# Optimization experiments

Hardware: AMD Instinct MI355X
Metric: run time of the kernel (lower is better)

Reference implementation:

```python
import jax, jax.numpy as jnp
import numpy as np

N = 20000       # nodes
E = 160000      # edges (avg degree 8)
NFEAT = 512
NHID = 512
NCLASS = 64
NLAYERS = 4


def setup_inputs() -> dict:
    key = jax.random.key(0)
    ks = jax.random.split(key, 9)
    s = 0.05
    x = jax.random.normal(ks[0], (N, NFEAT), dtype=jnp.float32)
    edge_index = jax.random.randint(ks[1], (2, E), 0, N, dtype=jnp.int64)
    W_enc = jax.random.normal(ks[2], (NFEAT, NHID), dtype=jnp.float32) * s
    b_enc = jnp.zeros((NHID,), dtype=jnp.float32)
    W_convs = jax.random.normal(ks[3], (NLAYERS, NHID, NHID), dtype=jnp.float32) * s
    b_convs = jnp.zeros((NLAYERS, NHID), dtype=jnp.float32)
    W_dec = jax.random.normal(ks[4], (NHID, NCLASS), dtype=jnp.float32) * s
    b_dec = jnp.zeros((NCLASS,), dtype=jnp.float32)
    return {"x": x, "edge_index": edge_index, "W_enc": W_enc, "b_enc": b_enc,
            "W_convs": W_convs, "b_convs": b_convs, "W_dec": W_dec, "b_dec": b_dec}


def reference(x, edge_index, W_enc, b_enc, W_convs, b_convs, W_dec, b_dec):
    n = x.shape[0]
    loops = jnp.arange(n, dtype=edge_index.dtype)
    # GCNConv adds self-loops, then sym-normalizes: D^-1/2 (A+I) D^-1/2
    src = jnp.concatenate([edge_index[0], loops])  # [E+N]
    dst = jnp.concatenate([edge_index[1], loops])  # [E+N]
    deg = jax.ops.segment_sum(jnp.ones_like(dst, dtype=x.dtype), dst, num_segments=N)
    dinv = jnp.where(deg > 0, jax.lax.rsqrt(deg), jnp.zeros_like(deg))
    norm = (dinv[src] * dinv[dst])[:, None]  # [E+N, 1]

    # encoder: relu(Linear)
    h = jax.nn.relu(x @ W_enc + b_enc)

    def gcn_step(h, wb):
        W, b = wb
        hW = h @ W                                   # [N, H]
        msg = hW[src] * norm                         # gather + scale
        agg = jax.ops.segment_sum(msg, dst, num_segments=N)  # scatter-add
        return jax.nn.relu(agg + b), None            # bias after aggregation (PyG)

    h, _ = jax.lax.scan(gcn_step, h, (W_convs, b_convs))

    # decoder (dropout p=0 in eval -> identity)
    return h @ W_dec + b_dec
```

## Files before the change

### kernel.cpp

```cpp
#include <hip/hip_runtime.h>

#define N_NODES 20000
#define E_EDGES 160000
#define NFEAT   512
#define NHID    512
#define NCLASS  64
#define NLAYERS 4

#define SCAN_CHUNK 1024
#define NBLK ((N_NODES + SCAN_CHUNK - 1) / SCAN_CHUNK)
#define CNT_BLOCKS ((E_EDGES + 255) / 256)
#define CVT_BLOCKS ((N_NODES * NFEAT) / 2048)

using bf16x8 = __attribute__((ext_vector_type(8))) short;
using f32x4  = __attribute__((ext_vector_type(4))) float;
using u16x8  = __attribute__((ext_vector_type(8))) unsigned short;

__device__ __forceinline__ unsigned short f2bf(float f) {
    union { float f; unsigned int u; } v; v.f = f;
    unsigned int u = v.u + 0x7FFFu + ((v.u >> 16) & 1u);
    return (unsigned short)(u >> 16);
}
__device__ __forceinline__ float bf2f(unsigned short h) {
    union { unsigned int u; float f; } v; v.u = ((unsigned int)h) << 16;
    return v.f;
}
__device__ __forceinline__ void gl2lds16(const void* gptr, void* lptr) {
    __builtin_amdgcn_global_load_lds(
        (const __attribute__((address_space(1))) unsigned int*)gptr,
        (__attribute__((address_space(3))) unsigned int*)lptr,
        16, 0, 0);
}

__global__ __launch_bounds__(256) void prep_all(const int* __restrict__ dst,
                                                int* __restrict__ counts,
                                                int* __restrict__ bsums,
                                                const float* __restrict__ W_enc,
                                                const float* __restrict__ W_convs,
                                                const float* __restrict__ W_dec,
                                                unsigned short* __restrict__ WencT,
                                                unsigned short* __restrict__ WcvT,
                                                unsigned short* __restrict__ WdecT,
                                                const float* __restrict__ x,
                                                unsigned short* __restrict__ Xbf) {
    __shared__ int bins[NBLK];
    __shared__ float tile[32][33];
    const int b = blockIdx.x, t = threadIdx.x;

    if (b < CNT_BLOCKS) {
        if (t < NBLK) bins[t] = 0;
        __syncthreads();
        const int e = b * 256 + t;
        if (e < E_EDGES) {
            const int d = dst[e];
            atomicAdd(&counts[d], 1);
            atomicAdd(&bins[d >> 10], 1);
        }
        __syncthreads();
        if (t < NBLK && bins[t]) atomicAdd(&bsums[t], bins[t]);
        return;
    }

    if (b >= CNT_BLOCKS + 6 * 256) {
        const int cid = b - CNT_BLOCKS - 6 * 256;
        const size_t base = (size_t)cid * 2048 + (size_t)t * 8;
        const float4 f0 = *(const float4*)(x + base);
        const float4 f1 = *(const float4*)(x + base + 4);
        u16x8 pk;
        pk[0] = f2bf(f0.x); pk[1] = f2bf(f0.y);
        pk[2] = f2bf(f0.z); pk[3] = f2bf(f0.w);
        pk[4] = f2bf(f1.x); pk[5] = f2bf(f1.y);
        pk[6] = f2bf(f1.z); pk[7] = f2bf(f1.w);
        *(u16x8*)(Xbf + base) = pk;
        return;
    }

    const int bid = b - CNT_BLOCKS;
    const int id  = bid >> 8;
    const int rem = bid & 255;
    const int n0  = (rem & 15) * 32;
    const int k0  = (rem >> 4) * 32;
    const float* W; unsigned short* WT; int N;
    const int K = 512;
    if (id == 0)            { W = W_enc; WT = WencT; N = NHID; }
    else if (id <= NLAYERS) { W = W_convs + (size_t)(id - 1) * NHID * NHID;
                              WT = WcvT  + (size_t)(id - 1) * NHID * NHID; N = NHID; }
    else                    { W = W_dec; WT = WdecT; N = NCLASS; }
    if (n0 >= N) return;
    const int tx = t & 31, ty = t >> 5;
#pragma unroll
    for (int i = 0; i < 32; i += 8)
        tile[ty + i][tx] = W[(size_t)(k0 + ty + i) * N + n0 + tx];
    __syncthreads();
#pragma unroll
    for (int i = 0; i < 32; i += 8)
        WT[(size_t)(n0 + ty + i) * K + k0 + tx] = f2bf(tile[tx][ty + i]);
}

__global__ __launch_bounds__(256) void write_rowptr(const int* __restrict__ counts,
                                                    const int* __restrict__ bsums,
                                                    int* __restrict__ row_ptr,
                                                    int* __restrict__ cursor,
                                                    float* __restrict__ dinv) {
    __shared__ int part[256];
    __shared__ int boff_s;
    const int b = blockIdx.x, t = threadIdx.x;

    if (t < 64) {
        int v = (t < NBLK && t < b) ? bsums[t] : 0;
        for (int off = 32; off > 0; off >>= 1) v += __shfl_xor(v, off, 64);
        if (t == 0) boff_s = v;
    }

    const int base = b * SCAN_CHUNK + t * 4;
    int c[4], s = 0;
    for (int i = 0; i < 4; ++i) {
        int idx = base + i;
        c[i] = (idx < N_NODES) ? counts[idx] : 0;
        s += c[i];
    }
    part[t] = s;
    __syncthreads();
    for (int off = 1; off < 256; off <<= 1) {
        int v = (t >= off) ? part[t - off] : 0;
        __syncthreads();
        part[t] += v;
        __syncthreads();
    }
    int run = boff_s + ((t == 0) ? 0 : part[t - 1]);
    for (int i = 0; i < 4; ++i) {
        int idx = base + i;
        if (idx < N_NODES) {
            row_ptr[idx] = run;
            cursor[idx]  = run;
            dinv[idx]    = rsqrtf((float)c[i] + 1.0f);
            run += c[i];
        }
    }
    if (b == 0 && t == 0) row_ptr[N_NODES] = E_EDGES;
}

__global__ __launch_bounds__(256) void csr_fill(const int* __restrict__ src,
                                                const int* __restrict__ dst,
                                                const float* __restrict__ dinv,
                                                int* __restrict__ cursor,
                                                int2* __restrict__ ew) {
    int e = blockIdx.x * 256 + threadIdx.x;
    if (e < E_EDGES) {
        int s = src[e], d = dst[e];
        int pos = atomicAdd(&cursor[d], 1);
        ew[pos] = make_int2(s, __float_as_int(dinv[s] * dinv[d]));
    }
    if (e < 8) ew[E_EDGES + e] = make_int2(0, 0);
}

template <int BM, int BN, int WR, int WC, bool RELU, bool HASBIAS, bool OUTBF16>
__global__ __launch_bounds__(256) void gemm_mfma(const unsigned short* __restrict__ A,
                                                 const unsigned short* __restrict__ BT,
                                                 const float* __restrict__ bias,
                                                 void* __restrict__ Cout,
                                                 int M, int N, int K) {
    constexpr int BK  = 64;
    constexpr int R   = BM / (16 * WR);
    constexpr int C   = BN / (16 * WC);
    constexpr int RA  = (BM * BK) / (256 * 8);
    constexpr int RB  = (BN * BK) / (256 * 8);
    constexpr int LPT = RA + RB;
    __shared__ unsigned short lA[2][BM * BK];
    __shared__ unsigned short lB[2][BN * BK];

    const int t    = threadIdx.x;
    const int lane = t & 63;
    const int wv   = t >> 6;
    const int wr   = wv / WC;
    const int wc   = wv % WC;
    const int lm   = lane & 15;
    const int quad = lane >> 4;
    const int sw   = lm & 7;

    const int MBLK = (M + BM - 1) / BM;
    const int NBN  = N / BN;
    int mblk, nblk;
    {
        const int i    = blockIdx.x;
        const int full = (MBLK / 8) * 8 * NBN;
        if (i < full) {
            const int g = i / (8 * NBN);
            const int l = i % (8 * NBN);
            mblk = g * 8 + (l & 7);
            nblk = l >> 3;
        } else {
            const int t2  = i - full;
            const int rem = MBLK - (MBLK / 8) * 8;
            mblk = (MBLK / 8) * 8 + t2 % rem;
            nblk = t2 / rem;
        }
    }
    const int m0 = mblk * BM;
    const int n0 = nblk * BN;

    f32x4 acc[R][C] = {};

    auto stage = [&](int s, int kt) {
#pragma unroll
        for (int i = 0; i < RA; ++i) {
            int idx = i * 256 + t;
            int row = idx >> 3;
            int c8  = idx & 7;
            int gr = m0 + row; if (gr >= M) gr = M - 1;
            gl2lds16(A + (size_t)gr * K + kt + (((c8 ^ (row & 7)) << 3)),
                     &lA[s][idx * 8]);
        }
#pragma unroll
        for (int i = 0; i < RB; ++i) {
            int idx = i * 256 + t;
            int row = idx >> 3;
            int c8  = idx & 7;
            gl2lds16(BT + (size_t)(n0 + row) * K + kt + (((c8 ^ (row & 7)) << 3)),
                     &lB[s][idx * 8]);
        }
    };

    stage(0, 0);
    int cur = 0;
    for (int kt = 0; kt < K; kt += BK) {
        if (kt + BK < K) {
            stage(cur ^ 1, kt + BK);
            asm volatile("s_waitcnt vmcnt(%0)" :: "i"(LPT) : "memory");
        } else {
            asm volatile("s_waitcnt vmcnt(0)" ::: "memory");
        }
        __builtin_amdgcn_sched_barrier(0);
        __builtin_amdgcn_s_barrier();

        bf16x8 af[R][2], bfr[C][2];
#pragma unroll
        for (int r = 0; r < R; ++r)
#pragma unroll
            for (int h = 0; h < 2; ++h)
                af[r][h] = *(const bf16x8*)
                    &lA[cur][(wr * R * 16 + r * 16 + lm) * BK +
                             (((h * 4 + quad) ^ sw) << 3)];
#pragma unroll
        for (int c = 0; c < C; ++c)
#pragma unroll
            for (int h = 0; h < 2; ++h)
                bfr[c][h] = *(const bf16x8*)
                    &lB[cur][(wc * C * 16 + c * 16 + lm) * BK +
                             (((h * 4 + quad) ^ sw) << 3)];
        asm volatile("s_waitcnt lgkmcnt(0)" ::: "memory");
        __builtin_amdgcn_sched_barrier(0);
#pragma unroll
        for (int h = 0; h < 2; ++h)
#pragma unroll
            for (int r = 0; r < R; ++r)
#pragma unroll
                for (int c = 0; c < C; ++c)
                    acc[r][c] = __builtin_amdgcn_mfma_f32_16x16x32_bf16(
                        af[r][h], bfr[c][h], acc[r][c], 0, 0, 0);
        __builtin_amdgcn_sched_barrier(0);
        __builtin_amdgcn_s_barrier();
        cur ^= 1;
    }

#pragma unroll
    for (int r = 0; r < R; ++r) {
#pragma unroll
        for (int c = 0; c < C; ++c) {
            const int colg = n0 + wc * C * 16 + c * 16 + lm;
            const float bb = HASBIAS ? bias[colg] : 0.0f;
            const int rowb = m0 + wr * R * 16 + r * 16 + quad * 4;
#pragma unroll
            for (int i = 0; i < 4; ++i) {
                const int rr = rowb + i;
                if (rr < M) {
                    float v = acc[r][c][i] + bb;
                    if (RELU) v = fmaxf(v, 0.0f);
                    if (OUTBF16)
                        ((unsigned short*)Cout)[(size_t)rr * N + colg] = f2bf(v);
                    else
                        ((float*)Cout)[(size_t)rr * N + colg] = v;
                }
            }
        }
    }
}

__global__ __launch_bounds__(256) void gcn_aggregate(const unsigned short* __restrict__ hW,
                                                     const int* __restrict__ row_ptr,
                                                     const int2* __restrict__ ew,
                                                     const float* __restrict__ dinv,
                                                     const float* __restrict__ bias,
                                                     unsigned short* __restrict__ out) {
    const int wv   = threadIdx.x >> 6;
    const int lane = threadIdx.x & 63;
    int d = blockIdx.x * 4 + wv;
    d = __builtin_amdgcn_readfirstlane(d);
    if (d >= N_NODES) return;
    const int beg = __builtin_amdgcn_readfirstlane(row_ptr[d]);
    const int end = __builtin_amdgcn_readfirstlane(row_ptr[d + 1]);
    const size_t foff = (size_t)lane * 8;

    const float di = dinv[d];
    const float sl = di * di;
    u16x8 sv = *(const u16x8*)(hW + (size_t)d * NHID + foff);
    float acc[8];
#pragma unroll
    for (int i = 0; i < 8; ++i) acc[i] = bf2f(sv[i]) * sl;

    for (int j = beg; j < end; j += 8) {
        int   sK[8];
        float wK[8];
        u16x8 v[8];
#pragma unroll
        for (int k = 0; k < 8; ++k) {
            const int jj = j + k;
            const int2 e = ew[jj];
            const bool valid = jj < end;
            sK[k] = valid ? e.x : 0;
            wK[k] = valid ? __int_as_float(e.y) : 0.0f;
        }
#pragma unroll
        for (int k = 0; k < 8; ++k)
            v[k] = *(const u16x8*)(hW + (size_t)sK[k] * NHID + foff);
#pragma unroll
        for (int k = 0; k < 8; ++k)
#pragma unroll
            for (int i = 0; i < 8; ++i)
                acc[i] += bf2f(v[k][i]) * wK[k];
    }

    const float4 b0v = *(const float4*)(bias + foff);
    const float4 b1v = *(const float4*)(bias + foff + 4);
    u16x8 r;
    r[0] = f2bf(fmaxf(acc[0] + b0v.x, 0.0f));
    r[1] = f2bf(fmaxf(acc[1] + b0v.y, 0.0f));
    r[2] = f2bf(fmaxf(acc[2] + b0v.z, 0.0f));
    r[3] = f2bf(fmaxf(acc[3] + b0v.w, 0.0f));
    r[4] = f2bf(fmaxf(acc[4] + b1v.x, 0.0f));
    r[5] = f2bf(fmaxf(acc[5] + b1v.y, 0.0f));
    r[6] = f2bf(fmaxf(acc[6] + b1v.z, 0.0f));
    r[7] = f2bf(fmaxf(acc[7] + b1v.w, 0.0f));
    *(u16x8*)(out + (size_t)d * NHID + foff) = r;
}

extern "C" void kernel_launch(void* const* d_in, const int* in_sizes, int n_in,
                              void* d_out, int out_size, void* d_ws, size_t ws_size,
                              hipStream_t stream) {
    const float* x       = (const float*)d_in[0];
    const int*   ei      = (const int*)d_in[1];
    const float* W_enc   = (const float*)d_in[2];
    const float* b_enc   = (const float*)d_in[3];
    const float* W_convs = (const float*)d_in[4];
    const float* b_convs = (const float*)d_in[5];
    const float* W_dec   = (const float*)d_in[6];
    const float* b_dec   = (const float*)d_in[7];
    float* out = (float*)d_out;

    const int* src = ei;
    const int* dst = ei + E_EDGES;

    char* ws = (char*)d_ws;
    auto alloc = [&](size_t bytes) {
        char* p = ws;
        ws += (bytes + 255) / 256 * 256;
        return p;
    };
    float* dinv     = (float*)alloc(N_NODES * 4);
    int*   counts   = (int*)  alloc((N_NODES + NBLK) * 4);
    int*   bsums    = counts + N_NODES;
    int*   row_ptr  = (int*)  alloc((N_NODES + 1) * 4);
    int*   cursor   = (int*)  alloc(N_NODES * 4);
    int2*  ew       = (int2*) alloc((E_EDGES + 8) * 8);
    unsigned short* WencT = (unsigned short*)alloc((size_t)NFEAT * NHID * 2);
    unsigned short* WcvT  = (unsigned short*)alloc((size_t)NLAYERS * NHID * NHID * 2);
    unsigned short* WdecT = (unsigned short*)alloc((size_t)NHID * NCLASS * 2);
    unsigned short* B1    = (unsigned short*)alloc((size_t)N_NODES * NHID * 2);
    unsigned short* B2    = (unsigned short*)alloc((size_t)N_NODES * NHID * 2);
    unsigned short* Xbf   = B2;

    hipMemsetAsync(counts, 0, (N_NODES + NBLK) * sizeof(int), stream);
    prep_all<<<CNT_BLOCKS + 6 * 256 + CVT_BLOCKS, 256, 0, stream>>>(
        dst, counts, bsums, W_enc, W_convs, W_dec, WencT, WcvT, WdecT, x, Xbf);
    write_rowptr<<<NBLK, 256, 0, stream>>>(counts, bsums, row_ptr, cursor, dinv);
    csr_fill<<<(E_EDGES + 255) / 256, 256, 0, stream>>>(src, dst, dinv, cursor, ew);

    const int MBLK64 = (N_NODES + 63) / 64;

    gemm_mfma<64, 128, 2, 2, true, true, true>
        <<<MBLK64 * (NHID / 128), 256, 0, stream>>>(
        Xbf, WencT, b_enc, B1, N_NODES, NHID, NFEAT);

    for (int L = 0; L < NLAYERS; ++L) {
        gemm_mfma<64, 128, 2, 2, false, false, true>
            <<<MBLK64 * (NHID / 128), 256, 0, stream>>>(
            B1, WcvT + (size_t)L * NHID * NHID, nullptr, B2, N_NODES, NHID, NHID);
        gcn_aggregate<<<(N_NODES + 3) / 4, 256, 0, stream>>>(
            B2, row_ptr, ew, dinv, b_convs + (size_t)L * NHID, B1);
    }

    gemm_mfma<64, 64, 2, 2, false, true, false>
        <<<MBLK64 * (NCLASS / 64), 256, 0, stream>>>(
        B1, WdecT, b_dec, out, N_NODES, NCLASS, NHID);
}
```

Measured before the change: 339.1 us.

## Keep full B panel resident in LDS and stream A fragments from global

Replaces the double-buffered LDS GEMM with a kernel that loads the whole K=512 slice of the weight panel (BN=64 columns, 64KB) into swizzled LDS once. Each wave then reads its own A-row fragments straight from global memory into registers, prefetching one k-step ahead. This removes per-k-tile barriers and the LDS staging of A. In exchange, A reads are uncoalesced 16-byte per-lane global loads with little latency hiding, and the large LDS footprint limits occupancy. Tile shapes change to 256x64 for the hidden GEMMs and 128x64 for the decoder.

```diff
diff --git a/kernel.cpp b/kernel.cpp
--- a/kernel.cpp
+++ b/kernel.cpp
@@ -154,29 +154,22 @@
     if (e < 8) ew[E_EDGES + e] = make_int2(0, 0);
 }
 
-template <int BM, int BN, int WR, int WC, bool RELU, bool HASBIAS, bool OUTBF16>
-__global__ __launch_bounds__(256) void gemm_mfma(const unsigned short* __restrict__ A,
+template <int R, int BN, bool RELU, bool HASBIAS, bool OUTBF16>
+__global__ __launch_bounds__(256) void gemm_bres(const unsigned short* __restrict__ A,
                                                  const unsigned short* __restrict__ BT,
                                                  const float* __restrict__ bias,
                                                  void* __restrict__ Cout,
-                                                 int M, int N, int K) {
-    constexpr int BK  = 64;
-    constexpr int R   = BM / (16 * WR);
-    constexpr int C   = BN / (16 * WC);
-    constexpr int RA  = (BM * BK) / (256 * 8);
-    constexpr int RB  = (BN * BK) / (256 * 8);
-    constexpr int LPT = RA + RB;
-    __shared__ unsigned short lA[2][BM * BK];
-    __shared__ unsigned short lB[2][BN * BK];
+                                                 int M, int N) {
+    constexpr int K  = 512;
+    constexpr int BM = 4 * R * 16;
+    constexpr int C  = BN / 16;
+    __shared__ unsigned short lB[BN * K];
 
     const int t    = threadIdx.x;
     const int lane = t & 63;
     const int wv   = t >> 6;
-    const int wr   = wv / WC;
-    const int wc   = wv % WC;
     const int lm   = lane & 15;
-    const int quad = lane >> 4;
-    const int sw   = lm & 7;
+    const int q    = lane >> 4;
 
     const int MBLK = (M + BM - 1) / BM;
     const int NBN  = N / BN;
@@ -191,7 +184,7 @@
             nblk = l >> 3;
         } else {
             const int t2  = i - full;
-            const int rem = MBLK - (MBLK / 8) * 8;
+            const int rem = MBLK & 7;
             mblk = (MBLK / 8) * 8 + t2 % rem;
             nblk = t2 / rem;
         }
@@ -199,77 +192,61 @@
     const int m0 = mblk * BM;
     const int n0 = nblk * BN;
 
+#pragma unroll
+    for (int i = 0; i < (BN * 64) / 256; ++i) {
+        const int idx = i * 256 + t;
+        const int row = idx >> 6;
+        const int c64 = idx & 63;
+        const int g   = (c64 & ~7) | ((c64 & 7) ^ (row & 7));
+        gl2lds16(BT + (size_t)(n0 + row) * K + g * 8, &lB[idx * 8]);
+    }
+    __syncthreads();
+
+    const unsigned short* ap[R];
+#pragma unroll
+    for (int r = 0; r < R; ++r) {
+        int gr = m0 + wv * R * 16 + r * 16 + lm;
+        if (gr >= M) gr = M - 1;
+        ap[r] = A + (size_t)gr * K + q * 8;
+    }
+
     f32x4 acc[R][C] = {};
-
-    auto stage = [&](int s, int kt) {
-#pragma unroll
-        for (int i = 0; i < RA; ++i) {
-            int idx = i * 256 + t;
-            int row = idx >> 3;
-            int c8  = idx & 7;
-            int gr = m0 + row; if (gr >= M) gr = M - 1;
-            gl2lds16(A + (size_t)gr * K + kt + (((c8 ^ (row & 7)) << 3)),
-                     &lA[s][idx * 8]);
-        }
-#pragma unroll
-        for (int i = 0; i < RB; ++i) {
-            int idx = i * 256 + t;
-            int row = idx >> 3;
-            int c8  = idx & 7;
-            gl2lds16(BT + (size_t)(n0 + row) * K + kt + (((c8 ^ (row & 7)) << 3)),
-                     &lB[s][idx * 8]);
-        }
-    };
-
-    stage(0, 0);
-    int cur = 0;
-    for (int kt = 0; kt < K; kt += BK) {
-        if (kt + BK < K) {
-            stage(cur ^ 1, kt + BK);
-            asm volatile("s_waitcnt vmcnt(%0)" :: "i"(LPT) : "memory");
-        } else {
-            asm volatile("s_waitcnt vmcnt(0)" ::: "memory");
-        }
-        __builtin_amdgcn_sched_barrier(0);
-        __builtin_amdgcn_s_barrier();
-
-        bf16x8 af[R][2], bfr[C][2];
+    bf16x8 aC[R], aN[R];
+#pragma unroll
+    for (int r = 0; r < R; ++r) aC[r] = *(const bf16x8*)ap[r];
+
+    for (int kt = 0; kt < K; kt += 32) {
+        if (kt + 32 < K) {
+#pragma unroll
+            for (int r = 0; r < R; ++r)
+                aN[r] = *(const bf16x8*)(ap[r] + kt + 32);
+        }
+        bf16x8 bf[C];
+        const int cb = kt >> 3;
+#pragma unroll
+        for (int c = 0; c < C; ++c) {
+            const int row  = c * 16 + lm;
+            const int c64  = cb + q;
+            const int phys = (c64 & ~7) | ((c64 & 7) ^ (row & 7));
+            bf[c] = *(const bf16x8*)&lB[row * K + phys * 8];
+        }
 #pragma unroll
         for (int r = 0; r < R; ++r)
 #pragma unroll
-            for (int h = 0; h < 2; ++h)
-                af[r][h] = *(const bf16x8*)
-                    &lA[cur][(wr * R * 16 + r * 16 + lm) * BK +
-                             (((h * 4 + quad) ^ sw) << 3)];
-#pragma unroll
-        for (int c = 0; c < C; ++c)
-#pragma unroll
-            for (int h = 0; h < 2; ++h)
-                bfr[c][h] = *(const bf16x8*)
-                    &lB[cur][(wc * C * 16 + c * 16 + lm) * BK +
-                             (((h * 4 + quad) ^ sw) << 3)];
-        asm volatile("s_waitcnt lgkmcnt(0)" ::: "memory");
-        __builtin_amdgcn_sched_barrier(0);
-#pragma unroll
-        for (int h = 0; h < 2; ++h)
-#pragma unroll
-            for (int r = 0; r < R; ++r)
-#pragma unroll
-                for (int c = 0; c < C; ++c)
-                    acc[r][c] = __builtin_amdgcn_mfma_f32_16x16x32_bf16(
-                        af[r][h], bfr[c][h], acc[r][c], 0, 0, 0);
-        __builtin_amdgcn_sched_barrier(0);
-        __builtin_amdgcn_s_barrier();
-        cur ^= 1;
+            for (int c = 0; c < C; ++c)
+                acc[r][c] = __builtin_amdgcn_mfma_f32_16x16x32_bf16(
+                    aC[r], bf[c], acc[r][c], 0, 0, 0);
+#pragma unroll
+        for (int r = 0; r < R; ++r) aC[r] = aN[r];
     }
 
 #pragma unroll
     for (int r = 0; r < R; ++r) {
 #pragma unroll
         for (int c = 0; c < C; ++c) {
-            const int colg = n0 + wc * C * 16 + c * 16 + lm;
+            const int colg = n0 + c * 16 + lm;
             const float bb = HASBIAS ? bias[colg] : 0.0f;
-            const int rowb = m0 + wr * R * 16 + r * 16 + quad * 4;
+            const int rowb = m0 + wv * R * 16 + r * 16 + q * 4;
 #pragma unroll
             for (int i = 0; i < 4; ++i) {
                 const int rr = rowb + i;
@@ -385,21 +362,22 @@
     write_rowptr<<<NBLK, 256, 0, stream>>>(counts, bsums, row_ptr, cursor, dinv);
     csr_fill<<<(E_EDGES + 255) / 256, 256, 0, stream>>>(src, dst, dinv, cursor, ew);
 
-    const int MBLK64 = (N_NODES + 63) / 64;
-
-    gemm_mfma<64, 128, 2, 2, true, true, true>
-        <<<MBLK64 * (NHID / 128), 256, 0, stream>>>(
-        Xbf, WencT, b_enc, B1, N_NODES, NHID, NFEAT);
+    const int MBLK256 = (N_NODES + 255) / 256;
+    const int MBLK128 = (N_NODES + 127) / 128;
+
+    gemm_bres<4, 64, true, true, true>
+        <<<MBLK256 * (NHID / 64), 256, 0, stream>>>(
+        Xbf, WencT, b_enc, B1, N_NODES, NHID);
 
     for (int L = 0; L < NLAYERS; ++L) {
-        gemm_mfma<64, 128, 2, 2, false, false, true>
-            <<<MBLK64 * (NHID / 128), 256, 0, stream>>>(
-            B1, WcvT + (size_t)L * NHID * NHID, nullptr, B2, N_NODES, NHID, NHID);
+        gemm_bres<4, 64, false, false, true>
+            <<<MBLK256 * (NHID / 64), 256, 0, stream>>>(
+            B1, WcvT + (size_t)L * NHID * NHID, nullptr, B2, N_NODES, NHID);
         gcn_aggregate<<<(N_NODES + 3) / 4, 256, 0, stream>>>(
             B2, row_ptr, ew, dinv, b_convs + (size_t)L * NHID, B1);
     }
 
-    gemm_mfma<64, 64, 2, 2, false, true, false>
-        <<<MBLK64 * (NCLASS / 64), 256, 0, stream>>>(
-        B1, WdecT, b_dec, out, N_NODES, NCLASS, NHID);
-}
+    gemm_bres<2, 64, false, true, false>
+        <<<MBLK128 * (NCLASS / 64), 256, 0, stream>>>(
+        B1, WdecT, b_dec, out, N_NODES, NCLASS);
+}
```

Result: slower. 407.8 us (+20.3%).
